# Kernel optimization log

Measured on AMD Instinct MI355X. Metric: run time of the kernel, lower is better.

Reference implementation:

```python
import jax, jax.numpy as jnp
import numpy as np

KERNELS = (3, 5, 7)
STEPS = 6
DMAX = 80.0
EPS = 1e-6


def unfold_neighbors(x, k):
    # x: (B,1,H,W) -> (B,k*k,H,W), zero-padded, row-major kernel order (center = k*k//2)
    p = k // 2
    return jax.lax.conv_general_dilated_patches(
        x, (k, k), (1, 1), [(p, p), (p, p)],
        dimension_numbers=("NCHW", "OIHW", "NCHW"))


def normalize_affinity(A):
    # CSPN abs-sum normalization over the k^2 channel dim
    return A / (jnp.sum(jnp.abs(A), axis=1, keepdims=True) + EPS)


def setup_inputs() -> dict:
    key = jax.random.key(0)
    ks = jax.random.split(key, 8)
    B, H, W = 2, 352, 1216
    D0 = jax.random.uniform(ks[0], (B, 1, H, W), jnp.float32) * DMAX
    DL = jax.random.uniform(ks[1], (B, 1, H, W), jnp.float32) * DMAX
    ML = jax.random.uniform(ks[2], (B, 1, H, W), jnp.float32)
    A3 = jax.random.normal(ks[3], (B, 9, H, W), jnp.float32)
    A5 = jax.random.normal(ks[4], (B, 25, H, W), jnp.float32)
    A7 = jax.random.normal(ks[5], (B, 49, H, W), jnp.float32)
    sigma_raw = jax.random.normal(ks[6], (B, 3, H, W), jnp.float32)
    alpha = jax.random.uniform(ks[7], (B, 1, H, W), jnp.float32)
    return {"D0": D0, "DL": DL, "ML": ML, "A3": A3, "A5": A5, "A7": A7,
            "sigma_raw": sigma_raw, "alpha": alpha}


def reference(D0, DL, ML, A3, A5, A7, sigma_raw, alpha):
    A_list = [normalize_affinity(A) for A in (A3, A5, A7)]
    sigma = jax.nn.softmax(sigma_raw, axis=1)  # KernelGate: convex mix over kernels
    m = (ML > 0.5).astype(D0.dtype)            # ML = (ML > 0).float()
    a = jnp.clip(alpha, 0.0, 1.0)

    def step(Dt, _):
        mix = jnp.zeros_like(Dt)
        for idx, k in enumerate(KERNELS):
            Ak = A_list[idx]
            patches = unfold_neighbors(Dt, k)          # (B,k*k,H,W)
            c = (k * k) // 2
            w_c = Ak[:, c:c + 1]
            p_c = patches[:, c:c + 1]
            Dk = jnp.sum(Ak * patches, axis=1, keepdims=True) + w_c * (D0 - p_c)
            mix = mix + sigma[:, idx:idx + 1] * Dk
        Dt = (1.0 - a * m) * mix + a * m * DL          # use_sparse anchoring
        Dt = jnp.clip(Dt, 0.0, DMAX)
        return Dt, None

    Dt, _ = jax.lax.scan(step, D0, None, length=STEPS)
    return Dt
```

## Files before the change

kernel.cpp:

```cpp
#include <hip/hip_runtime.h>

namespace {
constexpr int kB = 2;
constexpr int kH = 352;
constexpr int kW = 1216;
constexpr int kHW = kH * kW;
constexpr int kN = kB * kHW;
constexpr float kDmax = 80.0f;
constexpr float kEps = 1e-6f;
constexpr int kBlock = 256;
constexpr int kBlockP = 128;
}

typedef _Float16 half_t;
typedef __attribute__((ext_vector_type(4))) _Float16 half4;
typedef __attribute__((ext_vector_type(8))) _Float16 half8;

__device__ half_t g_Wh[(size_t)48 * kN];
__device__ float  g_Q[kN];
__device__ float  g_ping[kN];

__device__ __forceinline__ float4 ld4(const float* p) { return *(const float4*)p; }
__device__ __forceinline__ float4 f4add(float4 a, float4 b) {
    return make_float4(a.x + b.x, a.y + b.y, a.z + b.z, a.w + b.w);
}
__device__ __forceinline__ float4 f4mul(float4 a, float4 b) {
    return make_float4(a.x * b.x, a.y * b.y, a.z * b.z, a.w * b.w);
}
__device__ __forceinline__ float4 f4fma(float4 a, float4 b, float4 c) {
    return make_float4(fmaf(a.x, b.x, c.x), fmaf(a.y, b.y, c.y),
                       fmaf(a.z, b.z, c.z), fmaf(a.w, b.w, c.w));
}
__device__ __forceinline__ float4 f4abs(float4 a) {
    return make_float4(fabsf(a.x), fabsf(a.y), fabsf(a.z), fabsf(a.w));
}
__device__ __forceinline__ float4 f4max(float4 a, float4 b) {
    return make_float4(fmaxf(a.x, b.x), fmaxf(a.y, b.y),
                       fmaxf(a.z, b.z), fmaxf(a.w, b.w));
}
__device__ __forceinline__ half4 toh4(float4 v) {
    half4 h;
    h[0] = (half_t)v.x; h[1] = (half_t)v.y; h[2] = (half_t)v.z; h[3] = (half_t)v.w;
    return h;
}
__device__ __forceinline__ float4 tof4(half4 h) {
    return make_float4((float)h[0], (float)h[1], (float)h[2], (float)h[3]);
}

__global__ __launch_bounds__(kBlockP) void prep_kernel(
    const float* __restrict__ D0, const float* __restrict__ DL,
    const float* __restrict__ ML, const float* __restrict__ A3,
    const float* __restrict__ A5, const float* __restrict__ A7,
    const float* __restrict__ SG, const float* __restrict__ AL)
{
    __shared__ half_t sh7[49 * kBlockP * 4];
    __shared__ half_t sh5[25 * kBlockP * 4];

    int tid = threadIdx.x;
    int t = blockIdx.x * kBlockP + tid;
    int p = t * 4;
    int b = p / kHW;
    int rem = p - b * kHW;
    int sb = tid * 4;

    const float* a3p = A3 + (size_t)b * 9 * kHW + rem;
    const float* a5p = A5 + (size_t)b * 25 * kHW + rem;
    const float* a7p = A7 + (size_t)b * 49 * kHW + rem;
    const float* sgp = SG + (size_t)b * 3 * kHW + rem;

    float4 zero = make_float4(0.f, 0.f, 0.f, 0.f);

    float4 s7v = zero, c7v = zero;
#pragma unroll
    for (int ch = 0; ch < 6; ++ch) {
        float4 buf[8];
#pragma unroll
        for (int j = 0; j < 8; ++j) buf[j] = ld4(a7p + (size_t)(ch * 8 + j) * kHW);
#pragma unroll
        for (int j = 0; j < 8; ++j) {
            int c = ch * 8 + j;
            if (c == 24) c7v = buf[j];
            s7v = f4add(s7v, f4abs(buf[j]));
            *(half4*)(&sh7[c * (kBlockP * 4) + sb]) = toh4(buf[j]);
        }
    }
    {
        float4 l = ld4(a7p + (size_t)48 * kHW);
        s7v = f4add(s7v, f4abs(l));
        *(half4*)(&sh7[48 * (kBlockP * 4) + sb]) = toh4(l);
    }

    float4 s5v = zero, c5v = zero;
#pragma unroll
    for (int ch = 0; ch < 3; ++ch) {
        float4 buf[8];
#pragma unroll
        for (int j = 0; j < 8; ++j) buf[j] = ld4(a5p + (size_t)(ch * 8 + j) * kHW);
#pragma unroll
        for (int j = 0; j < 8; ++j) {
            int c = ch * 8 + j;
            if (c == 12) c5v = buf[j];
            s5v = f4add(s5v, f4abs(buf[j]));
            *(half4*)(&sh5[c * (kBlockP * 4) + sb]) = toh4(buf[j]);
        }
    }
    {
        float4 l = ld4(a5p + (size_t)24 * kHW);
        s5v = f4add(s5v, f4abs(l));
        *(half4*)(&sh5[24 * (kBlockP * 4) + sb]) = toh4(l);
    }

    float4 a3r[9];
    float4 s3v = zero;
#pragma unroll
    for (int c = 0; c < 9; ++c) a3r[c] = ld4(a3p + (size_t)c * kHW);
#pragma unroll
    for (int c = 0; c < 9; ++c) s3v = f4add(s3v, f4abs(a3r[c]));

    float4 g0 = ld4(sgp);
    float4 g1 = ld4(sgp + kHW);
    float4 g2 = ld4(sgp + 2 * kHW);
    float4 mx = f4max(g0, f4max(g1, g2));
    float4 e0 = make_float4(expf(g0.x - mx.x), expf(g0.y - mx.y), expf(g0.z - mx.z), expf(g0.w - mx.w));
    float4 e1 = make_float4(expf(g1.x - mx.x), expf(g1.y - mx.y), expf(g1.z - mx.z), expf(g1.w - mx.w));
    float4 e2 = make_float4(expf(g2.x - mx.x), expf(g2.y - mx.y), expf(g2.z - mx.z), expf(g2.w - mx.w));
    float4 einv = make_float4(1.f / (e0.x + e1.x + e2.x), 1.f / (e0.y + e1.y + e2.y),
                              1.f / (e0.z + e1.z + e2.z), 1.f / (e0.w + e1.w + e2.w));

    float4 alv = ld4(AL + p);
    float4 ml  = ld4(ML + p);
    float4 al = make_float4(fminf(fmaxf(alv.x, 0.f), 1.f), fminf(fmaxf(alv.y, 0.f), 1.f),
                            fminf(fmaxf(alv.z, 0.f), 1.f), fminf(fmaxf(alv.w, 0.f), 1.f));
    float4 mk = make_float4(ml.x > 0.5f ? 1.f : 0.f, ml.y > 0.5f ? 1.f : 0.f,
                            ml.z > 0.5f ? 1.f : 0.f, ml.w > 0.5f ? 1.f : 0.f);
    float4 g = f4mul(al, mk);
    float4 omg = make_float4(1.f - g.x, 1.f - g.y, 1.f - g.z, 1.f - g.w);

    float4 w3 = make_float4(omg.x * e0.x * einv.x / (s3v.x + kEps), omg.y * e0.y * einv.y / (s3v.y + kEps),
                            omg.z * e0.z * einv.z / (s3v.z + kEps), omg.w * e0.w * einv.w / (s3v.w + kEps));
    float4 w5 = make_float4(omg.x * e1.x * einv.x / (s5v.x + kEps), omg.y * e1.y * einv.y / (s5v.y + kEps),
                            omg.z * e1.z * einv.z / (s5v.z + kEps), omg.w * e1.w * einv.w / (s5v.w + kEps));
    float4 w7 = make_float4(omg.x * e2.x * einv.x / (s7v.x + kEps), omg.y * e2.y * einv.y / (s7v.y + kEps),
                            omg.z * e2.z * einv.z / (s7v.z + kEps), omg.w * e2.w * einv.w / (s7v.w + kEps));

    {
        float4 d0 = ld4(D0 + p);
        float4 dl = ld4(DL + p);
        float4 cw = f4fma(w3, a3r[4], f4fma(w5, c5v, f4mul(w7, c7v)));
        *(float4*)(&g_Q[p]) = f4fma(cw, d0, f4mul(g, dl));
    }

    int oi = 0;
#pragma unroll
    for (int i = 0; i < 49; ++i) {
        int dy = i / 7 - 3, dx = i % 7 - 3;
        if (dy == 0 && dx == 0) continue;
        float4 a7v = tof4(*(const half4*)(&sh7[i * (kBlockP * 4) + sb]));
        float4 wv = f4mul(w7, a7v);
        if (dy >= -2 && dy <= 2 && dx >= -2 && dx <= 2) {
            float4 a5v = tof4(*(const half4*)(&sh5[((dy + 2) * 5 + (dx + 2)) * (kBlockP * 4) + sb]));
            wv = f4fma(w5, a5v, wv);
        }
        if (dy >= -1 && dy <= 1 && dx >= -1 && dx <= 1)
            wv = f4fma(w3, a3r[(dy + 1) * 3 + (dx + 1)], wv);
        *(half4*)(&g_Wh[(size_t)oi * kN + p]) = toh4(wv);
        ++oi;
    }
}

__global__ __launch_bounds__(kBlock) void step_kernel(
    const float* __restrict__ Din_ext, float* __restrict__ Dout_ext,
    int src_g, int dst_g)
{
    const float* Din = src_g ? g_ping : Din_ext;
    float* Dout = dst_g ? g_ping : Dout_ext;

    int t = blockIdx.x * kBlock + threadIdx.x;
    int p = t * 8;
    int b = p / kHW;
    int rem = p - b * kHW;
    int y = rem / kW;
    int x0 = rem - y * kW;
    const float* dinb = Din + (size_t)b * kHW;

    float acc[8];
    {
        float4 q0 = ld4(&g_Q[p]);
        float4 q1 = ld4(&g_Q[p + 4]);
        acc[0] = q0.x; acc[1] = q0.y; acc[2] = q0.z; acc[3] = q0.w;
        acc[4] = q1.x; acc[5] = q1.y; acc[6] = q1.z; acc[7] = q1.w;
    }

    int oi = 0;
#pragma unroll
    for (int dy = -3; dy <= 3; ++dy) {
        int ny = y + dy;
        bool rv = (ny >= 0) && (ny < kH);
        if (!rv) { oi += (dy == 0) ? 6 : 7; continue; }
        const float* dr = dinb + ny * kW;

        float rowv[16];
#pragma unroll
        for (int s = 0; s < 4; ++s) {
            int xb = x0 + (s - 1) * 4;
            float4 v = (xb >= 0 && xb + 3 < kW) ? ld4(dr + xb)
                                                : make_float4(0.f, 0.f, 0.f, 0.f);
            rowv[s * 4 + 0] = v.x; rowv[s * 4 + 1] = v.y;
            rowv[s * 4 + 2] = v.z; rowv[s * 4 + 3] = v.w;
        }
#pragma unroll
        for (int dx = -3; dx <= 3; ++dx) {
            if (dy == 0 && dx == 0) continue;
            half8 w = *(const half8*)(&g_Wh[(size_t)oi * kN + p]);
#pragma unroll
            for (int j = 0; j < 8; ++j)
                acc[j] = fmaf((float)w[j], rowv[4 + j + dx], acc[j]);
            ++oi;
        }
    }

#pragma unroll
    for (int j = 0; j < 8; ++j)
        acc[j] = fminf(fmaxf(acc[j], 0.f), kDmax);
    *(float4*)(&Dout[p])     = make_float4(acc[0], acc[1], acc[2], acc[3]);
    *(float4*)(&Dout[p + 4]) = make_float4(acc[4], acc[5], acc[6], acc[7]);
}

extern "C" void kernel_launch(void* const* d_in, const int* in_sizes, int n_in,
                              void* d_out, int out_size, void* d_ws, size_t ws_size,
                              hipStream_t stream) {
    const float* D0 = (const float*)d_in[0];
    const float* DL = (const float*)d_in[1];
    const float* ML = (const float*)d_in[2];
    const float* A3 = (const float*)d_in[3];
    const float* A5 = (const float*)d_in[4];
    const float* A7 = (const float*)d_in[5];
    const float* SG = (const float*)d_in[6];
    const float* AL = (const float*)d_in[7];
    float* out = (float*)d_out;

    dim3 gridP(kN / 4 / kBlockP);
    dim3 gridO(kN / 8 / kBlock);

    prep_kernel<<<gridP, dim3(kBlockP), 0, stream>>>(D0, DL, ML, A3, A5, A7, SG, AL);

    step_kernel<<<gridO, dim3(kBlock), 0, stream>>>(D0, nullptr, 0, 1);
    step_kernel<<<gridO, dim3(kBlock), 0, stream>>>(nullptr, out, 1, 0);
    step_kernel<<<gridO, dim3(kBlock), 0, stream>>>(out, nullptr, 0, 1);
    step_kernel<<<gridO, dim3(kBlock), 0, stream>>>(nullptr, out, 1, 0);
    step_kernel<<<gridO, dim3(kBlock), 0, stream>>>(out, nullptr, 0, 1);
    step_kernel<<<gridO, dim3(kBlock), 0, stream>>>(nullptr, out, 1, 0);
}
```

Baseline: 193.5 us.

## Fuse first propagation step into prep kernel and resize step grid

The prep kernel now also runs the first propagation step. It reads D0 neighbours, accumulates with the freshly computed fp32 weights while writing the fp16 weights, and stores the clamped result to the ping buffer, so one step kernel launch and its pass over the weight array are dropped. The step kernels now use a fixed 512-block grid, each block covering 209 eight-pixel units, and the extra threads exit early. Risks are more register pressure in prep and idle lanes per block. The first step now uses fp32 weights rather than the rounded fp16 ones, so results differ slightly.

```diff
diff --git a/kernel.cpp b/kernel.cpp
--- a/kernel.cpp
+++ b/kernel.cpp
@@ -10,6 +10,8 @@
 constexpr float kEps = 1e-6f;
 constexpr int kBlock = 256;
 constexpr int kBlockP = 128;
+constexpr int kStepGrid = 512;
+constexpr int kUnitsPerBlk = 209;
 }
 
 typedef _Float16 half_t;
@@ -61,12 +63,15 @@
     int p = t * 4;
     int b = p / kHW;
     int rem = p - b * kHW;
+    int y = rem / kW;
+    int x0 = rem - y * kW;
     int sb = tid * 4;
 
     const float* a3p = A3 + (size_t)b * 9 * kHW + rem;
     const float* a5p = A5 + (size_t)b * 25 * kHW + rem;
     const float* a7p = A7 + (size_t)b * 49 * kHW + rem;
     const float* sgp = SG + (size_t)b * 3 * kHW + rem;
+    const float* d0b = D0 + (size_t)b * kHW;
 
     float4 zero = make_float4(0.f, 0.f, 0.f, 0.f);
 
@@ -143,39 +148,66 @@
     float4 w7 = make_float4(omg.x * e2.x * einv.x / (s7v.x + kEps), omg.y * e2.y * einv.y / (s7v.y + kEps),
                             omg.z * e2.z * einv.z / (s7v.z + kEps), omg.w * e2.w * einv.w / (s7v.w + kEps));
 
-    {
-        float4 d0 = ld4(D0 + p);
-        float4 dl = ld4(DL + p);
-        float4 cw = f4fma(w3, a3r[4], f4fma(w5, c5v, f4mul(w7, c7v)));
-        *(float4*)(&g_Q[p]) = f4fma(cw, d0, f4mul(g, dl));
-    }
-
+    float4 d0 = ld4(D0 + p);
+    float4 dl = ld4(DL + p);
+    float4 cw = f4fma(w3, a3r[4], f4fma(w5, c5v, f4mul(w7, c7v)));
+    float4 Qv = f4fma(cw, d0, f4mul(g, dl));
+    *(float4*)(&g_Q[p]) = Qv;
+
+    float acc[4] = {Qv.x, Qv.y, Qv.z, Qv.w};
     int oi = 0;
 #pragma unroll
-    for (int i = 0; i < 49; ++i) {
-        int dy = i / 7 - 3, dx = i % 7 - 3;
-        if (dy == 0 && dx == 0) continue;
-        float4 a7v = tof4(*(const half4*)(&sh7[i * (kBlockP * 4) + sb]));
-        float4 wv = f4mul(w7, a7v);
-        if (dy >= -2 && dy <= 2 && dx >= -2 && dx <= 2) {
-            float4 a5v = tof4(*(const half4*)(&sh5[((dy + 2) * 5 + (dx + 2)) * (kBlockP * 4) + sb]));
-            wv = f4fma(w5, a5v, wv);
-        }
-        if (dy >= -1 && dy <= 1 && dx >= -1 && dx <= 1)
-            wv = f4fma(w3, a3r[(dy + 1) * 3 + (dx + 1)], wv);
-        *(half4*)(&g_Wh[(size_t)oi * kN + p]) = toh4(wv);
-        ++oi;
-    }
+    for (int dy = -3; dy <= 3; ++dy) {
+        int ny = y + dy;
+        bool rv = (ny >= 0) && (ny < kH);
+        float rowv[12];
+        if (rv) {
+            const float* dr = d0b + ny * kW;
+#pragma unroll
+            for (int s = 0; s < 3; ++s) {
+                int xb = x0 + (s - 1) * 4;
+                float4 v = (xb >= 0 && xb + 3 < kW) ? ld4(dr + xb) : zero;
+                rowv[s * 4 + 0] = v.x; rowv[s * 4 + 1] = v.y;
+                rowv[s * 4 + 2] = v.z; rowv[s * 4 + 3] = v.w;
+            }
+        } else {
+#pragma unroll
+            for (int s = 0; s < 12; ++s) rowv[s] = 0.f;
+        }
+#pragma unroll
+        for (int dx = -3; dx <= 3; ++dx) {
+            if (dy == 0 && dx == 0) continue;
+            int i = (dy + 3) * 7 + (dx + 3);
+            float4 wv = f4mul(w7, tof4(*(const half4*)(&sh7[i * (kBlockP * 4) + sb])));
+            if (dy >= -2 && dy <= 2 && dx >= -2 && dx <= 2)
+                wv = f4fma(w5, tof4(*(const half4*)(&sh5[((dy + 2) * 5 + (dx + 2)) * (kBlockP * 4) + sb])), wv);
+            if (dy >= -1 && dy <= 1 && dx >= -1 && dx <= 1)
+                wv = f4fma(w3, a3r[(dy + 1) * 3 + (dx + 1)], wv);
+            *(half4*)(&g_Wh[(size_t)oi * kN + p]) = toh4(wv);
+            acc[0] = fmaf(wv.x, rowv[4 + 0 + dx], acc[0]);
+            acc[1] = fmaf(wv.y, rowv[4 + 1 + dx], acc[1]);
+            acc[2] = fmaf(wv.z, rowv[4 + 2 + dx], acc[2]);
+            acc[3] = fmaf(wv.w, rowv[4 + 3 + dx], acc[3]);
+            ++oi;
+        }
+    }
+    float4 o;
+    o.x = fminf(fmaxf(acc[0], 0.f), kDmax);
+    o.y = fminf(fmaxf(acc[1], 0.f), kDmax);
+    o.z = fminf(fmaxf(acc[2], 0.f), kDmax);
+    o.w = fminf(fmaxf(acc[3], 0.f), kDmax);
+    *(float4*)(&g_ping[p]) = o;
 }
 
 __global__ __launch_bounds__(kBlock) void step_kernel(
     const float* __restrict__ Din_ext, float* __restrict__ Dout_ext,
     int src_g, int dst_g)
 {
+    if (threadIdx.x >= kUnitsPerBlk) return;
     const float* Din = src_g ? g_ping : Din_ext;
     float* Dout = dst_g ? g_ping : Dout_ext;
 
-    int t = blockIdx.x * kBlock + threadIdx.x;
+    int t = blockIdx.x * kUnitsPerBlk + threadIdx.x;
     int p = t * 8;
     int b = p / kHW;
     int rem = p - b * kHW;
@@ -240,14 +272,13 @@
     float* out = (float*)d_out;
 
     dim3 gridP(kN / 4 / kBlockP);
-    dim3 gridO(kN / 8 / kBlock);
+    dim3 gridS(kStepGrid);
 
     prep_kernel<<<gridP, dim3(kBlockP), 0, stream>>>(D0, DL, ML, A3, A5, A7, SG, AL);
 
-    step_kernel<<<gridO, dim3(kBlock), 0, stream>>>(D0, nullptr, 0, 1);
-    step_kernel<<<gridO, dim3(kBlock), 0, stream>>>(nullptr, out, 1, 0);
-    step_kernel<<<gridO, dim3(kBlock), 0, stream>>>(out, nullptr, 0, 1);
-    step_kernel<<<gridO, dim3(kBlock), 0, stream>>>(nullptr, out, 1, 0);
-    step_kernel<<<gridO, dim3(kBlock), 0, stream>>>(out, nullptr, 0, 1);
-    step_kernel<<<gridO, dim3(kBlock), 0, stream>>>(nullptr, out, 1, 0);
-}
+    step_kernel<<<gridS, dim3(kBlock), 0, stream>>>(nullptr, out, 1, 0);
+    step_kernel<<<gridS, dim3(kBlock), 0, stream>>>(out, nullptr, 0, 1);
+    step_kernel<<<gridS, dim3(kBlock), 0, stream>>>(nullptr, out, 1, 0);
+    step_kernel<<<gridS, dim3(kBlock), 0, stream>>>(out, nullptr, 0, 1);
+    step_kernel<<<gridS, dim3(kBlock), 0, stream>>>(nullptr, out, 1, 0);
+}
```

New measurement: 189.5 us. -2.1%, faster.
